# Optimization experiments

Hardware: AMD Instinct MI355X
Metric: run time of the kernel (lower is better)

Reference implementation:

```python
import jax, jax.numpy as jnp
import numpy as np

B, SQ, SK, D, H, HD = 2, 2048, 2048, 1024, 16, 64


def setup_inputs() -> dict:
    key = jax.random.key(0)
    ks = jax.random.split(key, 10)
    s = 1.0 / np.sqrt(D)  # keep activations well-scaled
    return {
        "x": jax.random.normal(ks[0], (B, SQ, D), jnp.float32),
        "encoder_output": jax.random.normal(ks[1], (B, SK, D), jnp.float32),
        "Wq": jax.random.normal(ks[2], (H, D, HD), jnp.float32) * s,
        "bq": jax.random.normal(ks[3], (H, HD), jnp.float32) * 0.01,
        "Wk": jax.random.normal(ks[4], (H, D, HD), jnp.float32) * s,
        "bk": jax.random.normal(ks[5], (H, HD), jnp.float32) * 0.01,
        "Wv": jax.random.normal(ks[6], (H, D, HD), jnp.float32) * s,
        "bv": jax.random.normal(ks[7], (H, HD), jnp.float32) * 0.01,
        "Wo": jax.random.normal(ks[8], (D, D), jnp.float32) * s,
        "bo": jax.random.normal(ks[9], (D,), jnp.float32) * 0.01,
    }


def reference(x, encoder_output, Wq, bq, Wk, bk, Wv, bv, Wo, bo):
    # Batched per-head projections (equivalent to the per-head nn.Linear loop).
    q = jnp.einsum('bsd,hde->bhse', x, Wq) + bq[None, :, None, :]              # [B,H,SQ,HD]
    k = jnp.einsum('bsd,hde->bhse', encoder_output, Wk) + bk[None, :, None, :]  # [B,H,SK,HD]
    v = jnp.einsum('bsd,hde->bhse', encoder_output, Wv) + bv[None, :, None, :]  # [B,H,SK,HD]
    scale = 1.0 / jnp.sqrt(jnp.asarray(HD, q.dtype))
    scores = jnp.einsum('bhqe,bhke->bhqk', q, k) * scale                        # [B,H,SQ,SK]
    attn = jax.nn.softmax(scores, axis=-1)
    out = jnp.einsum('bhqk,bhke->bhqe', attn, v)                                # [B,H,SQ,HD]
    # concat heads along feature dim (head order matches torch.cat order)
    out = out.transpose(0, 2, 1, 3).reshape(out.shape[0], out.shape[2], -1)     # [B,SQ,D]
    # final linear; dropout is identity in eval mode
    return out @ Wo + bo
```

## Files before the change

### kernel.cpp

```cpp
#include <hip/hip_runtime.h>


typedef unsigned short u16;
typedef __bf16 bf16x8 __attribute__((ext_vector_type(8)));
typedef float f32x4 __attribute__((ext_vector_type(4)));
typedef float f32x16 __attribute__((ext_vector_type(16)));
typedef unsigned u32x2 __attribute__((ext_vector_type(2)));

#define B_ 2
#define SQ_ 2048
#define SK_ 2048
#define D_ 1024
#define H_ 16
#define HD_ 64

__device__ __forceinline__ u16 f2bf(float f) {
  union { float f; unsigned u; } c; c.f = f;
  unsigned u = c.u;
  return (u16)((u + 0x7fffu + ((u >> 16) & 1u)) >> 16);
}
__device__ __forceinline__ float bf2f(u16 h) {
  union { unsigned u; float f; } c; c.u = ((unsigned)h) << 16;
  return c.f;
}
__device__ __forceinline__ unsigned pack_bf16(float lo, float hi) {
  union { __bf16 h[2]; unsigned u; } c;
  c.h[0] = (__bf16)lo;
  c.h[1] = (__bf16)hi;
  return c.u;
}

#define GLOAD_LDS16(gp, lp)                                                  \
  __builtin_amdgcn_global_load_lds(                                          \
      (const __attribute__((address_space(1))) void*)(gp),                   \
      (__attribute__((address_space(3))) void*)(lp), 16, 0, 0)

__global__ __launch_bounds__(256) void cast2_f32_bf16(const float* __restrict__ x,
                                                      const float* __restrict__ enc,
                                                      u16* __restrict__ xb,
                                                      u16* __restrict__ eb) {
  const float* in = blockIdx.z ? enc : x;
  u16* out = blockIdx.z ? eb : xb;
  int i = blockIdx.x * 256 + threadIdx.x;
  float4 v = ((const float4*)in)[i];
  uint2 p;
  p.x = (unsigned)f2bf(v.x) | ((unsigned)f2bf(v.y) << 16);
  p.y = (unsigned)f2bf(v.z) | ((unsigned)f2bf(v.w) << 16);
  ((uint2*)out)[i] = p;
}

__global__ __launch_bounds__(256) void wqkv_trans(const float* __restrict__ Wq,
                                                  const float* __restrict__ Wk,
                                                  const float* __restrict__ Wv,
                                                  u16* __restrict__ out) {
  __shared__ float tile[64][65];
  const int mat = blockIdx.z >> 4, head = blockIdx.z & 15;
  const float* W = (mat == 0) ? Wq : (mat == 1 ? Wk : Wv);
  const float* ib = W + (long)head * 65536;
  u16* ob = out + ((long)mat << 20) + (long)head * 65536;
  int r0 = blockIdx.y << 6;
  int tid = threadIdx.x;
#pragma unroll
  for (int i = 0; i < 16; ++i) {
    int idx = tid + (i << 8);
    int r = idx >> 6, c = idx & 63;
    tile[r][c] = ib[(long)(r0 + r) * 64 + c];
  }
  __syncthreads();
#pragma unroll
  for (int i = 0; i < 16; ++i) {
    int idx = tid + (i << 8);
    int cc = idx >> 6, rr = idx & 63;
    ob[(long)cc * 1024 + (r0 + rr)] = f2bf(tile[rr][cc]);
  }
}

__global__ __launch_bounds__(256) void transpose_to_bf16(const float* __restrict__ in,
                                                         u16* __restrict__ out,
                                                         int R, int C,
                                                         long ibs, long obs) {
  __shared__ float tile[64][65];
  const float* ib = in + (long)blockIdx.z * ibs;
  u16* ob = out + (long)blockIdx.z * obs;
  int r0 = blockIdx.y << 6, c0 = blockIdx.x << 6;
  int tid = threadIdx.x;
#pragma unroll
  for (int i = 0; i < 16; ++i) {
    int idx = tid + (i << 8);
    int r = idx >> 6, c = idx & 63;
    tile[r][c] = ib[(long)(r0 + r) * C + (c0 + c)];
  }
  __syncthreads();
#pragma unroll
  for (int i = 0; i < 16; ++i) {
    int idx = tid + (i << 8);
    int cc = idx >> 6, rr = idx & 63;
    ob[(long)(c0 + cc) * R + (r0 + rr)] = f2bf(tile[rr][cc]);
  }
}

__global__ __launch_bounds__(256) void gemm_qkv(const u16* __restrict__ xb,
                                                const u16* __restrict__ eb,
                                                const u16* __restrict__ Wt3,
                                                const float* __restrict__ bq,
                                                const float* __restrict__ bk,
                                                const float* __restrict__ bv,
                                                u16* __restrict__ qws,
                                                u16* __restrict__ kws,
                                                u16* __restrict__ vT) {
  constexpr int M = 2048, N = 1024, K = 1024;
  __shared__ __align__(16) u16 As[128 * 32];
  __shared__ __align__(16) u16 Bs[128 * 32];
  const int tid = threadIdx.x;
  const int lane = tid & 63;
  const int wid = tid >> 6;
  const int l16 = lane & 15, quad = lane >> 4;
  const int wm = wid >> 1, wn = wid & 1;
  const int bn0g = blockIdx.x << 7;
  const int seg = bn0g >> 10;
  const int bn0 = bn0g & (N - 1);
  const int bm0 = blockIdx.y << 7;
  const u16* A = (seg == 0) ? xb : eb;
  const u16* Wt = Wt3 + ((long)seg << 20);
  const float* bias = (seg == 0) ? bq : (seg == 1 ? bk : bv);
  const long abase = (long)blockIdx.z * M * K;

  f32x4 acc[4][4];
#pragma unroll
  for (int i = 0; i < 4; ++i)
#pragma unroll
    for (int j = 0; j < 4; ++j) acc[i][j] = f32x4{0.f, 0.f, 0.f, 0.f};

  const int r0 = tid >> 2;
  const int c0s = (tid & 3) << 3;
  const u16* agp = A + abase + (long)(bm0 + r0) * K + c0s;
  const u16* bgp = Wt + (long)(bn0 + r0) * K + c0s;
  u16* alp = As + tid * 8;
  u16* blp = Bs + tid * 8;

  for (int k0 = 0; k0 < K; k0 += 32) {
    GLOAD_LDS16(agp + k0, alp);
    GLOAD_LDS16(agp + k0 + (long)64 * K, alp + 2048);
    GLOAD_LDS16(bgp + k0, blp);
    GLOAD_LDS16(bgp + k0 + (long)64 * K, blp + 2048);
    __syncthreads();
    bf16x8 af[4], bfr[4];
#pragma unroll
    for (int mi = 0; mi < 4; ++mi)
      af[mi] = *(const bf16x8*)(As + (wm * 64 + mi * 16 + l16) * 32 + quad * 8);
#pragma unroll
    for (int ni = 0; ni < 4; ++ni)
      bfr[ni] = *(const bf16x8*)(Bs + (wn * 64 + ni * 16 + l16) * 32 + quad * 8);
#pragma unroll
    for (int mi = 0; mi < 4; ++mi)
#pragma unroll
      for (int ni = 0; ni < 4; ++ni)
        acc[mi][ni] = __builtin_amdgcn_mfma_f32_16x16x32_bf16(af[mi], bfr[ni],
                                                              acc[mi][ni], 0, 0, 0);
    __syncthreads();
  }

  float bv4[4];
#pragma unroll
  for (int ni = 0; ni < 4; ++ni) bv4[ni] = bias[bn0 + wn * 64 + ni * 16 + l16];

  if (seg == 2) {
    const long zb = (long)blockIdx.z * N * M;
#pragma unroll
    for (int mi = 0; mi < 4; ++mi)
#pragma unroll
      for (int ni = 0; ni < 4; ++ni) {
        int colg = bn0 + wn * 64 + ni * 16 + l16;
        int rowg = bm0 + wm * 64 + mi * 16 + (quad << 2);
        ushort4 pk = make_ushort4(f2bf(acc[mi][ni][0] + bv4[ni]),
                                  f2bf(acc[mi][ni][1] + bv4[ni]),
                                  f2bf(acc[mi][ni][2] + bv4[ni]),
                                  f2bf(acc[mi][ni][3] + bv4[ni]));
        *(ushort4*)(vT + zb + (long)colg * M + rowg) = pk;
      }
  } else {
    u16* outp = seg ? kws : qws;
    const long cbase = (long)blockIdx.z * M * N;
#pragma unroll
    for (int mi = 0; mi < 4; ++mi)
#pragma unroll
      for (int ni = 0; ni < 4; ++ni)
#pragma unroll
        for (int r = 0; r < 4; ++r) {
          int row = bm0 + wm * 64 + mi * 16 + (quad << 2) + r;
          int col = bn0 + wn * 64 + ni * 16 + l16;
          outp[cbase + (long)row * N + col] = f2bf(acc[mi][ni][r] + bv4[ni]);
        }
  }
}

__global__ __launch_bounds__(256) void gemm_final(const u16* __restrict__ A,
                                                  const u16* __restrict__ Wt,
                                                  const float* __restrict__ bias,
                                                  float* __restrict__ C) {
  constexpr int M = 2048, N = 1024, K = 1024;
  __shared__ __align__(16) u16 As[64 * 32];
  __shared__ __align__(16) u16 Bs[128 * 32];
  const int tid = threadIdx.x;
  const int lane = tid & 63;
  const int wid = tid >> 6;
  const int l16 = lane & 15, quad = lane >> 4;
  const int bn0 = blockIdx.x << 7, bm0 = blockIdx.y << 6;

  f32x4 acc[4][2];
#pragma unroll
  for (int i = 0; i < 4; ++i)
#pragma unroll
    for (int j = 0; j < 2; ++j) acc[i][j] = f32x4{0.f, 0.f, 0.f, 0.f};

  const int r0 = tid >> 2;
  const int c0s = (tid & 3) << 3;
  const long abase = (long)blockIdx.z * M * K;
  const u16* agp = A + abase + (long)(bm0 + r0) * K + c0s;
  const u16* bgp = Wt + (long)(bn0 + r0) * K + c0s;
  u16* alp = As + tid * 8;
  u16* blp = Bs + tid * 8;

  for (int k0 = 0; k0 < K; k0 += 32) {
    GLOAD_LDS16(agp + k0, alp);
    GLOAD_LDS16(bgp + k0, blp);
    GLOAD_LDS16(bgp + k0 + (long)64 * K, blp + 2048);
    __syncthreads();
    bf16x8 af[4], bfr[2];
#pragma unroll
    for (int mi = 0; mi < 4; ++mi)
      af[mi] = *(const bf16x8*)(As + (mi * 16 + l16) * 32 + quad * 8);
#pragma unroll
    for (int ni = 0; ni < 2; ++ni)
      bfr[ni] = *(const bf16x8*)(Bs + (wid * 32 + ni * 16 + l16) * 32 + quad * 8);
#pragma unroll
    for (int mi = 0; mi < 4; ++mi)
#pragma unroll
      for (int ni = 0; ni < 2; ++ni)
        acc[mi][ni] = __builtin_amdgcn_mfma_f32_16x16x32_bf16(af[mi], bfr[ni],
                                                              acc[mi][ni], 0, 0, 0);
    __syncthreads();
  }

  float bv2[2];
#pragma unroll
  for (int ni = 0; ni < 2; ++ni) bv2[ni] = bias[bn0 + wid * 32 + ni * 16 + l16];
  const long cbase = (long)blockIdx.z * M * N;
#pragma unroll
  for (int mi = 0; mi < 4; ++mi)
#pragma unroll
    for (int ni = 0; ni < 2; ++ni)
#pragma unroll
      for (int r = 0; r < 4; ++r) {
        int row = bm0 + mi * 16 + (quad << 2) + r;
        int col = bn0 + wid * 32 + ni * 16 + l16;
        C[cbase + (long)row * N + col] = acc[mi][ni][r] + bv2[ni];
      }
}

#define ATTN_STAGE(bb)                                                        \
  do {                                                                        \
    GLOAD_LDS16(kp, Ks + ((bb) << 12) + tid * 8);                             \
    GLOAD_LDS16(kp + (long)32 * D_, Ks + ((bb) << 12) + 2048 + tid * 8);      \
    GLOAD_LDS16(vp, Vs + ((bb) << 12) + tid * 8);                             \
    GLOAD_LDS16(vp + (long)32 * SK_, Vs + ((bb) << 12) + 2048 + tid * 8);     \
  } while (0)

#define PV_KS(dd, k1, ks)                                                     \
  do {                                                                        \
    u32x2 sA = __builtin_amdgcn_permlane32_swap(dd[4 * (k1)],                 \
                                                dd[4 * (k1) + 2], false,      \
                                                false);                       \
    u32x2 sB = __builtin_amdgcn_permlane32_swap(dd[4 * (k1) + 1],             \
                                                dd[4 * (k1) + 3], false,      \
                                                false);                       \
    union { unsigned u[4]; bf16x8 v; } pa;                                    \
    pa.u[0] = sA[0]; pa.u[1] = sB[0]; pa.u[2] = sA[1]; pa.u[3] = sB[1];       \
    bf16x8 v0 = *(const bf16x8*)(Vb + ro0 + sw[ks]);                          \
    bf16x8 v1 = *(const bf16x8*)(Vb + 2048 + ro0 + sw[ks]);                   \
    o0 = __builtin_amdgcn_mfma_f32_32x32x16_bf16(pa.v, v0, o0, 0, 0, 0);      \
    o1 = __builtin_amdgcn_mfma_f32_32x32x16_bf16(pa.v, v1, o1, 0, 0, 0);      \
  } while (0)

__global__ __launch_bounds__(256, 2) void attn_flash(const u16* __restrict__ q,
                                                     const u16* __restrict__ k,
                                                     const u16* __restrict__ vT,
                                                     u16* __restrict__ ctx) {
  __shared__ __align__(16) u16 Ks[2 * 4096];
  __shared__ __align__(16) u16 Vs[2 * 4096];

  const int tid = threadIdx.x;
  const int lane = tid & 63;
  const int wid = tid >> 6;
  const int l31 = lane & 31, h5 = lane >> 5;
  const int h = blockIdx.y, b = blockIdx.z;
  const int q0w = (blockIdx.x << 7) + (wid << 5);

  bf16x8 qf[4];
  const u16* qp = q + ((long)(b * SQ_ + q0w + l31) * D_ + h * HD_ + 8 * h5);
#pragma unroll
  for (int j = 0; j < 4; ++j) qf[j] = *(const bf16x8*)(qp + 16 * j);

  const int srow = tid >> 3;
  const int ssw = ((tid & 7) ^ (srow & 7)) << 3;
  const u16* kp = k + ((long)(b * SK_ + srow) * D_ + h * HD_ + ssw);
  const u16* vp = vT + ((long)(b * D_ + h * HD_ + srow) * SK_ + ssw);

  const int ro0 = l31 << 6;
  int sw[4];
#pragma unroll
  for (int i = 0; i < 4; ++i) sw[i] = ((2 * i + h5) ^ (lane & 7)) << 3;

  f32x16 o0, o1;
#pragma unroll
  for (int i = 0; i < 16; ++i) { o0[i] = 0.f; o1[i] = 0.f; }
  float psA = 0.f, psB = 0.f;

  ATTN_STAGE(0);
  kp += (long)64 * D_;
  vp += 64;

  for (int c = 0; c < 32; ++c) {
    const int cur = c & 1;
    __syncthreads();
    if (c < 31) {
      ATTN_STAGE(cur ^ 1);
      kp += (long)64 * D_;
      vp += 64;
    }
    const u16* Kb = Ks + (cur << 12);
    const u16* Vb = Vs + (cur << 12);

    f32x16 s0, s1;
#pragma unroll
    for (int i = 0; i < 16; ++i) { s0[i] = 0.f; s1[i] = 0.f; }
    __builtin_amdgcn_s_setprio(1);
#pragma unroll
    for (int j = 0; j < 4; ++j) {
      bf16x8 kf0 = *(const bf16x8*)(Kb + ro0 + sw[j]);
      bf16x8 kf1 = *(const bf16x8*)(Kb + 2048 + ro0 + sw[j]);
      s0 = __builtin_amdgcn_mfma_f32_32x32x16_bf16(kf0, qf[j], s0, 0, 0, 0);
      s1 = __builtin_amdgcn_mfma_f32_32x32x16_bf16(kf1, qf[j], s1, 0, 0, 0);
    }
    __builtin_amdgcn_s_setprio(0);

    unsigned d0[8], d1[8];
#pragma unroll
    for (int g = 0; g < 8; ++g) {
      float a0 = __expf(s0[2 * g] * 0.125f);
      float a1 = __expf(s0[2 * g + 1] * 0.125f);
      float b0 = __expf(s1[2 * g] * 0.125f);
      float b1 = __expf(s1[2 * g + 1] * 0.125f);
      psA += a0 + a1;
      psB += b0 + b1;
      d0[g] = pack_bf16(a0, a1);
      d1[g] = pack_bf16(b0, b1);
    }

    __builtin_amdgcn_s_setprio(1);
    PV_KS(d0, 0, 0);
    PV_KS(d0, 1, 1);
    PV_KS(d1, 0, 2);
    PV_KS(d1, 1, 3);
    __builtin_amdgcn_s_setprio(0);
  }

  float ps = psA + psB;
  ps += __shfl_xor(ps, 32, 64);
  float inv = 1.f / ps;

#pragma unroll
  for (int r = 0; r < 16; ++r) {
    const int crow = (r & 3) + 8 * (r >> 2) + 4 * h5;
    float dq = __shfl(inv, crow, 64);
    long base = (long)(b * SQ_ + q0w + crow) * D_ + h * HD_ + l31;
    ctx[base] = f2bf(o0[r] * dq);
    ctx[base + 32] = f2bf(o1[r] * dq);
  }
}

extern "C" void kernel_launch(void* const* d_in, const int* in_sizes, int n_in,
                              void* d_out, int out_size, void* d_ws, size_t ws_size,
                              hipStream_t stream) {
  const float* x   = (const float*)d_in[0];
  const float* enc = (const float*)d_in[1];
  const float* Wq  = (const float*)d_in[2];
  const float* bq  = (const float*)d_in[3];
  const float* Wk  = (const float*)d_in[4];
  const float* bk  = (const float*)d_in[5];
  const float* Wv  = (const float*)d_in[6];
  const float* bv  = (const float*)d_in[7];
  const float* Wo  = (const float*)d_in[8];
  const float* bo  = (const float*)d_in[9];

  const long NE_X = (long)B_ * SQ_ * D_;
  const long NE_W = (long)D_ * D_;

  u16* outA = (u16*)d_out;
  u16* outB = outA + NE_X;
  u16* eb  = outB;
  u16* vTp = outA;

  u16* ws  = (u16*)d_ws;
  u16* WqT = ws;
  u16* WoT = WqT + 3 * NE_W;
  u16* qws = WoT + NE_W;
  u16* kws = qws + NE_X;
  u16* xb  = kws + NE_X;
  u16* ctx = xb;

  cast2_f32_bf16<<<dim3((unsigned)(NE_X / 4 / 256), 1, 2), 256, 0, stream>>>(x, enc, xb, eb);

  wqkv_trans<<<dim3(1, 16, 48), 256, 0, stream>>>(Wq, Wk, Wv, WqT);
  transpose_to_bf16<<<dim3(16, 16, 1), 256, 0, stream>>>(Wo, WoT, 1024, 1024, 0L, 0L);

  gemm_qkv<<<dim3(24, 16, 2), 256, 0, stream>>>(xb, eb, WqT, bq, bk, bv,
                                                qws, kws, vTp);

  attn_flash<<<dim3(SQ_ / 128, H_, B_), 256, 0, stream>>>(qws, kws, vTp, ctx);

  gemm_final<<<dim3(8, 32, 2), 256, 0, stream>>>(ctx, WoT, bo, (float*)d_out);
}
```

Before: 235.6 us.

## Software-pipeline QK^T of next tile with softmax and PV of current tile

Restructures the attention main loop so the QK^T MFMA for the next KV tile is issued before the exp/pack and PV MFMAs of the current tile. V gets a triple buffer so its tile stays live one iteration longer. The 1/sqrt(d) scale is folded into Q at load time, which removes a per-score multiply but rounds the scaled Q to bf16. The goal is to overlap the exp work with matrix work. In exchange it holds two sets of score registers, which raises register pressure, and uses more LDS.

Result: faster. 228.5 us (-3.0%).

```diff
diff --git a/kernel.cpp b/kernel.cpp
--- a/kernel.cpp
+++ b/kernel.cpp
@@ -258,15 +258,43 @@
       }
 }
 
-#define ATTN_STAGE(bb)                                                        \
+
+#define ATTN_STAGE(kbase, vbase)                                              \
   do {                                                                        \
-    GLOAD_LDS16(kp, Ks + ((bb) << 12) + tid * 8);                             \
-    GLOAD_LDS16(kp + (long)32 * D_, Ks + ((bb) << 12) + 2048 + tid * 8);      \
-    GLOAD_LDS16(vp, Vs + ((bb) << 12) + tid * 8);                             \
-    GLOAD_LDS16(vp + (long)32 * SK_, Vs + ((bb) << 12) + 2048 + tid * 8);     \
+    GLOAD_LDS16(kp, (kbase) + tid * 8);                                       \
+    GLOAD_LDS16(kp + (long)32 * D_, (kbase) + 2048 + tid * 8);                \
+    GLOAD_LDS16(vp, (vbase) + tid * 8);                                       \
+    GLOAD_LDS16(vp + (long)32 * SK_, (vbase) + 2048 + tid * 8);               \
+    kp += (long)64 * D_;                                                      \
+    vp += 64;                                                                 \
   } while (0)
 
-#define PV_KS(dd, k1, ks)                                                     \
+#define QK_BLOCK(Kb, sx0, sx1)                                                \
+  do {                                                                        \
+    _Pragma("unroll") for (int i = 0; i < 16; ++i) { sx0[i] = 0.f; sx1[i] = 0.f; } \
+    _Pragma("unroll") for (int j = 0; j < 4; ++j) {                           \
+      bf16x8 kf0 = *(const bf16x8*)((Kb) + ro0 + sw[j]);                      \
+      bf16x8 kf1 = *(const bf16x8*)((Kb) + 2048 + ro0 + sw[j]);               \
+      sx0 = __builtin_amdgcn_mfma_f32_32x32x16_bf16(kf0, qf[j], sx0, 0, 0, 0);\
+      sx1 = __builtin_amdgcn_mfma_f32_32x32x16_bf16(kf1, qf[j], sx1, 0, 0, 0);\
+    }                                                                         \
+  } while (0)
+
+#define EXPD(sx0, sx1)                                                        \
+  do {                                                                        \
+    _Pragma("unroll") for (int g = 0; g < 8; ++g) {                           \
+      float a0 = __expf(sx0[2 * g]);                                          \
+      float a1 = __expf(sx0[2 * g + 1]);                                      \
+      float b0 = __expf(sx1[2 * g]);                                          \
+      float b1 = __expf(sx1[2 * g + 1]);                                      \
+      psA += a0 + a1;                                                         \
+      psB += b0 + b1;                                                         \
+      d0[g] = pack_bf16(a0, a1);                                              \
+      d1[g] = pack_bf16(b0, b1);                                              \
+    }                                                                         \
+  } while (0)
+
+#define PV_KS(Vb, dd, k1, ks)                                                 \
   do {                                                                        \
     u32x2 sA = __builtin_amdgcn_permlane32_swap(dd[4 * (k1)],                 \
                                                 dd[4 * (k1) + 2], false,      \
@@ -276,10 +304,18 @@
                                                 false);                       \
     union { unsigned u[4]; bf16x8 v; } pa;                                    \
     pa.u[0] = sA[0]; pa.u[1] = sB[0]; pa.u[2] = sA[1]; pa.u[3] = sB[1];       \
-    bf16x8 v0 = *(const bf16x8*)(Vb + ro0 + sw[ks]);                          \
-    bf16x8 v1 = *(const bf16x8*)(Vb + 2048 + ro0 + sw[ks]);                   \
+    bf16x8 v0 = *(const bf16x8*)((Vb) + ro0 + sw[ks]);                        \
+    bf16x8 v1 = *(const bf16x8*)((Vb) + 2048 + ro0 + sw[ks]);                 \
     o0 = __builtin_amdgcn_mfma_f32_32x32x16_bf16(pa.v, v0, o0, 0, 0, 0);      \
     o1 = __builtin_amdgcn_mfma_f32_32x32x16_bf16(pa.v, v1, o1, 0, 0, 0);      \
+  } while (0)
+
+#define PV4(Vb)                                                               \
+  do {                                                                        \
+    PV_KS(Vb, d0, 0, 0);                                                      \
+    PV_KS(Vb, d0, 1, 1);                                                      \
+    PV_KS(Vb, d1, 0, 2);                                                      \
+    PV_KS(Vb, d1, 1, 3);                                                      \
   } while (0)
 
 __global__ __launch_bounds__(256, 2) void attn_flash(const u16* __restrict__ q,
@@ -287,7 +323,7 @@
                                                      const u16* __restrict__ vT,
                                                      u16* __restrict__ ctx) {
   __shared__ __align__(16) u16 Ks[2 * 4096];
-  __shared__ __align__(16) u16 Vs[2 * 4096];
+  __shared__ __align__(16) u16 Vs[3 * 4096];
 
   const int tid = threadIdx.x;
   const int lane = tid & 63;
@@ -299,7 +335,12 @@
   bf16x8 qf[4];
   const u16* qp = q + ((long)(b * SQ_ + q0w + l31) * D_ + h * HD_ + 8 * h5);
 #pragma unroll
-  for (int j = 0; j < 4; ++j) qf[j] = *(const bf16x8*)(qp + 16 * j);
+  for (int j = 0; j < 4; ++j) {
+    bf16x8 t = *(const bf16x8*)(qp + 16 * j);
+#pragma unroll
+    for (int e = 0; e < 8; ++e) t[e] = (__bf16)((float)t[e] * 0.125f);
+    qf[j] = t;
+  }
 
   const int srow = tid >> 3;
   const int ssw = ((tid & 7) ^ (srow & 7)) << 3;
@@ -311,59 +352,44 @@
 #pragma unroll
   for (int i = 0; i < 4; ++i) sw[i] = ((2 * i + h5) ^ (lane & 7)) << 3;
 
-  f32x16 o0, o1;
+  f32x16 o0, o1, sA0, sA1, sB0, sB1;
 #pragma unroll
   for (int i = 0; i < 16; ++i) { o0[i] = 0.f; o1[i] = 0.f; }
   float psA = 0.f, psB = 0.f;
-
-  ATTN_STAGE(0);
-  kp += (long)64 * D_;
-  vp += 64;
-
-  for (int c = 0; c < 32; ++c) {
-    const int cur = c & 1;
-    __syncthreads();
-    if (c < 31) {
-      ATTN_STAGE(cur ^ 1);
-      kp += (long)64 * D_;
-      vp += 64;
-    }
-    const u16* Kb = Ks + (cur << 12);
-    const u16* Vb = Vs + (cur << 12);
-
-    f32x16 s0, s1;
-#pragma unroll
-    for (int i = 0; i < 16; ++i) { s0[i] = 0.f; s1[i] = 0.f; }
-    __builtin_amdgcn_s_setprio(1);
-#pragma unroll
-    for (int j = 0; j < 4; ++j) {
-      bf16x8 kf0 = *(const bf16x8*)(Kb + ro0 + sw[j]);
-      bf16x8 kf1 = *(const bf16x8*)(Kb + 2048 + ro0 + sw[j]);
-      s0 = __builtin_amdgcn_mfma_f32_32x32x16_bf16(kf0, qf[j], s0, 0, 0, 0);
-      s1 = __builtin_amdgcn_mfma_f32_32x32x16_bf16(kf1, qf[j], s1, 0, 0, 0);
-    }
-    __builtin_amdgcn_s_setprio(0);
-
-    unsigned d0[8], d1[8];
-#pragma unroll
-    for (int g = 0; g < 8; ++g) {
-      float a0 = __expf(s0[2 * g] * 0.125f);
-      float a1 = __expf(s0[2 * g + 1] * 0.125f);
-      float b0 = __expf(s1[2 * g] * 0.125f);
-      float b1 = __expf(s1[2 * g + 1] * 0.125f);
-      psA += a0 + a1;
-      psB += b0 + b1;
-      d0[g] = pack_bf16(a0, a1);
-      d1[g] = pack_bf16(b0, b1);
-    }
-
-    __builtin_amdgcn_s_setprio(1);
-    PV_KS(d0, 0, 0);
-    PV_KS(d0, 1, 1);
-    PV_KS(d1, 0, 2);
-    PV_KS(d1, 1, 3);
-    __builtin_amdgcn_s_setprio(0);
-  }
+  unsigned d0[8], d1[8];
+
+  ATTN_STAGE(Ks, Vs);
+  ATTN_STAGE(Ks + 4096, Vs + 4096);
+  __syncthreads();
+  QK_BLOCK(Ks, sA0, sA1);
+
+  int viP = 0;
+  int viS = 2;
+
+  for (int tp = 0; tp < 30; tp += 2) {
+    __syncthreads();
+    ATTN_STAGE(Ks, Vs + viS * 4096);
+    viS = (viS == 2) ? 0 : viS + 1;
+    QK_BLOCK(Ks + 4096, sB0, sB1);
+    EXPD(sA0, sA1);
+    PV4(Vs + viP * 4096);
+    viP = (viP == 2) ? 0 : viP + 1;
+    __syncthreads();
+    ATTN_STAGE(Ks + 4096, Vs + viS * 4096);
+    viS = (viS == 2) ? 0 : viS + 1;
+    QK_BLOCK(Ks, sA0, sA1);
+    EXPD(sB0, sB1);
+    PV4(Vs + viP * 4096);
+    viP = (viP == 2) ? 0 : viP + 1;
+  }
+  __syncthreads();
+  QK_BLOCK(Ks + 4096, sB0, sB1);
+  EXPD(sA0, sA1);
+  PV4(Vs + viP * 4096);
+  viP = (viP == 2) ? 0 : viP + 1;
+  __syncthreads();
+  EXPD(sB0, sB1);
+  PV4(Vs + viP * 4096);
 
   float ps = psA + psB;
   ps += __shfl_xor(ps, 32, 64);
```
